# Kernel optimization log

Hardware: AMD Instinct MI355X
Metric: run time of the kernel (lower is better)

Reference implementation:

```python
import jax, jax.numpy as jnp
import numpy as np

L = 4096          # total packed tokens (B=1)
N_SEQ = 8         # number of packed sequences
SEQ = L // N_SEQ  # equal lengths of 512
H = 8
E = 64
NEG_BIAS = -10000.0  # matches torch.where(mask, 0, -10000.0)


def setup_inputs() -> dict:
    key = jax.random.key(0)
    kq, kk, kv = jax.random.split(key, 3)
    q = jax.random.normal(kq, (1, L, H, E), dtype=jnp.float32)
    k = jax.random.normal(kk, (1, L, H, E), dtype=jnp.float32)
    v = jax.random.normal(kv, (1, L, H, E), dtype=jnp.float32)
    # segment id per token; equivalent to lenghts=[512]*8 in the torch module
    seg_ids = (jnp.arange(L, dtype=jnp.int32) // SEQ).astype(jnp.int32)
    return {"q": q, "k": k, "v": v, "seg_ids": seg_ids}


def reference(q, k, v, seg_ids):
    # direct_attention: scores = (q @ k^T) * scale + block-diagonal bias; softmax; @ v
    scale = 1.0 / jnp.sqrt(jnp.asarray(E, dtype=q.dtype))
    # [B,H,L,L]
    scores = jnp.einsum('blhe,bmhe->bhlm', q, k) * scale
    # block-diagonal mask from segment ids (same as create_block_mask(lengths))
    same_block = seg_ids[:, None] == seg_ids[None, :]          # [L,L] bool
    bias = jnp.where(same_block, 0.0, NEG_BIAS).astype(q.dtype)  # additive bias, not -inf
    attn = jax.nn.softmax(scores + bias, axis=-1)
    out = jnp.einsum('bhlm,bmhe->blhe', attn, v)
    return out
```

## Files before the change

kernel.cpp:

```cpp
#include <hip/hip_runtime.h>
#include <cstdint>

#define NSEG 8
#define SEQ  512
#define NH   8
#define NE   64
#define KVB  64
#define QTILE 128
#define KVHALF 256
#define NCH 4
#define M2BIAS 24.0f
#define LOG2E  1.4426950408889634f
#define LDS_TOTAL 131072

typedef __attribute__((ext_vector_type(8)))  __bf16   bf16x8;
typedef __attribute__((ext_vector_type(16))) float    f32x16;
typedef __attribute__((ext_vector_type(4)))  uint32_t u32x4;

static __device__ __forceinline__ uint32_t cvtpk(float lo, float hi) {
    uint32_t r;
    asm("v_cvt_pk_bf16_f32 %0, %1, %2" : "=v"(r) : "v"(lo), "v"(hi));
    return r;
}
static __device__ __forceinline__ float exp2_fast(float x) {
    float r;
    asm("v_exp_f32 %0, %1" : "=v"(r) : "v"(x));
    return r;
}
static __device__ __forceinline__ f32x16 zero16() {
    f32x16 z;
#pragma unroll
    for (int i = 0; i < 16; ++i) z[i] = 0.0f;
    return z;
}

struct Pref {
    float4 k0, k1, k2, k3;
    float4 va0, va1, vb0, vb1;
};

static __device__ __forceinline__ void issue_loads(
    const float* __restrict__ kg, const float* __restrict__ vg,
    int kbase, int h, int tg, Pref& P)
{
    const int kr = tg >> 2, kc = (tg & 3) * 16;
    const float* ks = kg + (size_t)(kbase + kr) * (NH * NE) + h * NE + kc;
    P.k0 = *(const float4*)(ks);
    P.k1 = *(const float4*)(ks + 4);
    P.k2 = *(const float4*)(ks + 8);
    P.k3 = *(const float4*)(ks + 12);
    const int vr = (tg & 31) * 2, ve = (tg >> 5) * 8;
    const float* vs = vg + (size_t)(kbase + vr) * (NH * NE) + h * NE + ve;
    P.va0 = *(const float4*)(vs);
    P.va1 = *(const float4*)(vs + 4);
    P.vb0 = *(const float4*)(vs + NH * NE);
    P.vb1 = *(const float4*)(vs + NH * NE + 4);
}

static __device__ __forceinline__ void convert_store(
    char* ldsK, char* ldsV, int gc, int tg, const Pref& P)
{
    {
        const int kr = tg >> 2, kc2 = (tg & 3) * 32;
        const int swz = (kr & 7) << 4;
        char* dst = ldsK + gc * 8192 + kr * 128;
        u32x4 w0 = { cvtpk(P.k0.x, P.k0.y), cvtpk(P.k0.z, P.k0.w),
                     cvtpk(P.k1.x, P.k1.y), cvtpk(P.k1.z, P.k1.w) };
        u32x4 w1 = { cvtpk(P.k2.x, P.k2.y), cvtpk(P.k2.z, P.k2.w),
                     cvtpk(P.k3.x, P.k3.y), cvtpk(P.k3.z, P.k3.w) };
        *(u32x4*)(dst + ((kc2)      ^ swz)) = w0;
        *(u32x4*)(dst + ((kc2 + 16) ^ swz)) = w1;
    }
    {
        const int vr = (tg & 31) * 2, ve = (tg >> 5) * 8;
        float a[8] = { P.va0.x, P.va0.y, P.va0.z, P.va0.w,
                       P.va1.x, P.va1.y, P.va1.z, P.va1.w };
        float b[8] = { P.vb0.x, P.vb0.y, P.vb0.z, P.vb0.w,
                       P.vb1.x, P.vb1.y, P.vb1.z, P.vb1.w };
#pragma unroll
        for (int i = 0; i < 8; ++i) {
            const int e = ve + i;
            *(uint32_t*)(ldsV + e * 1024 + gc * 128 + ((vr * 2) ^ ((e & 7) << 4))) = cvtpk(a[i], b[i]);
        }
    }
}

__global__ __launch_bounds__(512, 2) void attn_fwd(
    const float* __restrict__ qg, const float* __restrict__ kg,
    const float* __restrict__ vg, float* __restrict__ outg)
{
    extern __shared__ __align__(16) char lds[];
    char* ldsK = lds;
    char* ldsV = lds + 65536;

    const int bid = blockIdx.x;
    const int seg = bid & 7;
    const int h   = (bid >> 3) & 7;
    const int qt  = bid >> 6;

    const int t    = threadIdx.x;
    const int lane = t & 63;
    const int wid  = t >> 6;
    const int wq   = wid & 3;
    const int kgp  = wid >> 2;
    const int tg   = t & 255;
    const int ql   = lane & 31;
    const int hi   = lane >> 5;

    const int qbase  = seg * SEQ + qt * QTILE + wq * 32;
    const int kvbase = seg * SEQ + kgp * KVHALF;
    const int gc0    = kgp * NCH;

    Pref Pa, Pb;
    issue_loads(kg, vg, kvbase,       h, tg, Pa);
    issue_loads(kg, vg, kvbase + KVB, h, tg, Pb);

    bf16x8 qf[4];
#pragma unroll
    for (int s = 0; s < 4; ++s) {
        const float* qp = qg + (size_t)(qbase + ql) * (NH * NE) + h * NE + s * 16 + hi * 8;
        float4 a = *(const float4*)qp;
        float4 b = *(const float4*)(qp + 4);
        u32x4 w = { cvtpk(a.x * 0.125f, a.y * 0.125f), cvtpk(a.z * 0.125f, a.w * 0.125f),
                    cvtpk(b.x * 0.125f, b.y * 0.125f), cvtpk(b.z * 0.125f, b.w * 0.125f) };
        qf[s] = __builtin_bit_cast(bf16x8, w);
    }

    convert_store(ldsK, ldsV, gc0 + 0, tg, Pa);
    issue_loads(kg, vg, kvbase + 2 * KVB, h, tg, Pa);
    convert_store(ldsK, ldsV, gc0 + 1, tg, Pb);
    issue_loads(kg, vg, kvbase + 3 * KVB, h, tg, Pb);
    convert_store(ldsK, ldsV, gc0 + 2, tg, Pa);
    convert_store(ldsK, ldsV, gc0 + 3, tg, Pb);
    __syncthreads();

    f32x16 o0 = zero16();
    f32x16 o1 = zero16();
    float lsum = 0.0f;

#pragma unroll 1
    for (int c = 0; c < NCH; ++c) {
        const int gc = gc0 + c;
        const char* bK = ldsK + gc * 8192;

        f32x16 sa = zero16();
        f32x16 sb = zero16();
#pragma unroll
        for (int s = 0; s < 4; ++s) {
            const int col = (s * 32 + hi * 16) ^ ((ql & 7) << 4);
            bf16x8 ka = *(const bf16x8*)(bK + ql * 128 + col);
            bf16x8 kb = *(const bf16x8*)(bK + (ql + 32) * 128 + col);
            sa = __builtin_amdgcn_mfma_f32_32x32x16_bf16(ka, qf[s], sa, 0, 0, 0);
            sb = __builtin_amdgcn_mfma_f32_32x32x16_bf16(kb, qf[s], sb, 0, 0, 0);
        }

#pragma unroll
        for (int r = 0; r < 16; ++r) {
            sa[r] = exp2_fast(fmaf(sa[r], LOG2E, -M2BIAS));
            sb[r] = exp2_fast(fmaf(sb[r], LOG2E, -M2BIAS));
        }
        float acc = 0.0f;
#pragma unroll
        for (int r = 0; r < 16; ++r) acc += sa[r] + sb[r];
        lsum += acc;

        uint32_t WA[2][4], WB[2][4];
#pragma unroll
        for (int r0 = 0; r0 < 4; ++r0) {
            WA[0][r0] = cvtpk(sa[4 * r0],     sa[4 * r0 + 1]);
            WB[0][r0] = cvtpk(sa[4 * r0 + 2], sa[4 * r0 + 3]);
            WA[1][r0] = cvtpk(sb[4 * r0],     sb[4 * r0 + 1]);
            WB[1][r0] = cvtpk(sb[4 * r0 + 2], sb[4 * r0 + 3]);
        }

#pragma unroll
        for (int ks = 0; ks < 4; ++ks) {
            const int kt = ks >> 1, g2 = (ks & 1) * 2;
            uint32_t Ua = hi ? WA[kt][g2 + 1] : WA[kt][g2];
            uint32_t Ub = hi ? WB[kt][g2 + 1] : WB[kt][g2];
            uint32_t Sa = hi ? WA[kt][g2]     : WA[kt][g2 + 1];
            uint32_t Sb = hi ? WB[kt][g2]     : WB[kt][g2 + 1];
            uint32_t Ra = __shfl_xor(Sa, 32);
            uint32_t Rb = __shfl_xor(Sb, 32);
            u32x4 pw = { hi ? Ra : Ua, hi ? Rb : Ub, hi ? Ua : Ra, hi ? Ub : Rb };
            bf16x8 pf = __builtin_bit_cast(bf16x8, pw);
            {
                const int e = ql;
                bf16x8 vb = *(const bf16x8*)(ldsV + e * 1024 + gc * 128 +
                                             ((ks * 32 + hi * 16) ^ ((e & 7) << 4)));
                o0 = __builtin_amdgcn_mfma_f32_32x32x16_bf16(pf, vb, o0, 0, 0, 0);
            }
            {
                const int e = 32 + ql;
                bf16x8 vb = *(const bf16x8*)(ldsV + e * 1024 + gc * 128 +
                                             ((ks * 32 + hi * 16) ^ ((e & 7) << 4)));
                o1 = __builtin_amdgcn_mfma_f32_32x32x16_bf16(pf, vb, o1, 0, 0, 0);
            }
        }
    }

    __syncthreads();
    float* ex = (float*)lds;
    if (kgp == 1) {
        float* p = ex + (size_t)(wq * 64 + lane) * 33;
#pragma unroll
        for (int r = 0; r < 16; ++r) { p[r] = o0[r]; p[16 + r] = o1[r]; }
        p[32] = lsum;
    }
    __syncthreads();
    if (kgp == 0) {
        const float* p = ex + (size_t)(wq * 64 + lane) * 33;
#pragma unroll
        for (int r = 0; r < 16; ++r) { o0[r] += p[r]; o1[r] += p[16 + r]; }
        lsum += p[32];

        const float ltot = lsum + __shfl_xor(lsum, 32);
        const float rinv = 1.0f / ltot;
#pragma unroll
        for (int r = 0; r < 16; ++r) {
            const int qlocal = (r & 3) + 8 * (r >> 2) + 4 * hi;
            const float scl = __shfl(rinv, qlocal);
            float* op = outg + (size_t)(qbase + qlocal) * (NH * NE) + h * NE + ql;
            op[0]  = o0[r] * scl;
            op[32] = o1[r] * scl;
        }
    }
}

extern "C" void kernel_launch(void* const* d_in, const int* in_sizes, int n_in,
                              void* d_out, int out_size, void* d_ws, size_t ws_size,
                              hipStream_t stream)
{
    (void)in_sizes; (void)n_in; (void)d_ws; (void)ws_size; (void)out_size;
    const float* q = (const float*)d_in[0];
    const float* k = (const float*)d_in[1];
    const float* v = (const float*)d_in[2];
    float* out = (float*)d_out;
    (void)hipFuncSetAttribute((const void*)attn_fwd,
                              hipFuncAttributeMaxDynamicSharedMemorySize, LDS_TOTAL);
    attn_fwd<<<dim3(NSEG * NH * (SEQ / QTILE)), dim3(512), LDS_TOTAL, stream>>>(q, k, v, out);
}
```

Before: 21.08 us.

## Split keys across four wave groups with 1024-thread blocks and single-shot loads

Doubles the block size to 1024 threads so four wave groups each handle a quarter of the 512 keys, halving the per-wave serial chunk loop. The staged, double-buffered K/V prefetch is replaced by one bulk load per thread into registers followed by a single LDS store. The final reduction now merges three partial outputs through LDS instead of one. This trades more register pressure and lower occupancy per CU for shorter per-wave critical paths, and the 12-group exchange region must still fit in LDS.

```diff
diff --git a/kernel.cpp b/kernel.cpp
--- a/kernel.cpp
+++ b/kernel.cpp
@@ -7,8 +7,9 @@
 #define NE   64
 #define KVB  64
 #define QTILE 128
-#define KVHALF 256
-#define NCH 4
+#define NKGP 4
+#define KEYS_PER_G (SEQ / NKGP)
+#define NCH (KEYS_PER_G / KVB)
 #define M2BIAS 24.0f
 #define LOG2E  1.4426950408889634f
 #define LDS_TOTAL 131072
@@ -34,58 +35,7 @@
     return z;
 }
 
-struct Pref {
-    float4 k0, k1, k2, k3;
-    float4 va0, va1, vb0, vb1;
-};
-
-static __device__ __forceinline__ void issue_loads(
-    const float* __restrict__ kg, const float* __restrict__ vg,
-    int kbase, int h, int tg, Pref& P)
-{
-    const int kr = tg >> 2, kc = (tg & 3) * 16;
-    const float* ks = kg + (size_t)(kbase + kr) * (NH * NE) + h * NE + kc;
-    P.k0 = *(const float4*)(ks);
-    P.k1 = *(const float4*)(ks + 4);
-    P.k2 = *(const float4*)(ks + 8);
-    P.k3 = *(const float4*)(ks + 12);
-    const int vr = (tg & 31) * 2, ve = (tg >> 5) * 8;
-    const float* vs = vg + (size_t)(kbase + vr) * (NH * NE) + h * NE + ve;
-    P.va0 = *(const float4*)(vs);
-    P.va1 = *(const float4*)(vs + 4);
-    P.vb0 = *(const float4*)(vs + NH * NE);
-    P.vb1 = *(const float4*)(vs + NH * NE + 4);
-}
-
-static __device__ __forceinline__ void convert_store(
-    char* ldsK, char* ldsV, int gc, int tg, const Pref& P)
-{
-    {
-        const int kr = tg >> 2, kc2 = (tg & 3) * 32;
-        const int swz = (kr & 7) << 4;
-        char* dst = ldsK + gc * 8192 + kr * 128;
-        u32x4 w0 = { cvtpk(P.k0.x, P.k0.y), cvtpk(P.k0.z, P.k0.w),
-                     cvtpk(P.k1.x, P.k1.y), cvtpk(P.k1.z, P.k1.w) };
-        u32x4 w1 = { cvtpk(P.k2.x, P.k2.y), cvtpk(P.k2.z, P.k2.w),
-                     cvtpk(P.k3.x, P.k3.y), cvtpk(P.k3.z, P.k3.w) };
-        *(u32x4*)(dst + ((kc2)      ^ swz)) = w0;
-        *(u32x4*)(dst + ((kc2 + 16) ^ swz)) = w1;
-    }
-    {
-        const int vr = (tg & 31) * 2, ve = (tg >> 5) * 8;
-        float a[8] = { P.va0.x, P.va0.y, P.va0.z, P.va0.w,
-                       P.va1.x, P.va1.y, P.va1.z, P.va1.w };
-        float b[8] = { P.vb0.x, P.vb0.y, P.vb0.z, P.vb0.w,
-                       P.vb1.x, P.vb1.y, P.vb1.z, P.vb1.w };
-#pragma unroll
-        for (int i = 0; i < 8; ++i) {
-            const int e = ve + i;
-            *(uint32_t*)(ldsV + e * 1024 + gc * 128 + ((vr * 2) ^ ((e & 7) << 4))) = cvtpk(a[i], b[i]);
-        }
-    }
-}
-
-__global__ __launch_bounds__(512, 2) void attn_fwd(
+__global__ __launch_bounds__(1024) void attn_fwd(
     const float* __restrict__ qg, const float* __restrict__ kg,
     const float* __restrict__ vg, float* __restrict__ outg)
 {
@@ -103,17 +53,26 @@
     const int wid  = t >> 6;
     const int wq   = wid & 3;
     const int kgp  = wid >> 2;
-    const int tg   = t & 255;
     const int ql   = lane & 31;
     const int hi   = lane >> 5;
 
-    const int qbase  = seg * SEQ + qt * QTILE + wq * 32;
-    const int kvbase = seg * SEQ + kgp * KVHALF;
-    const int gc0    = kgp * NCH;
-
-    Pref Pa, Pb;
-    issue_loads(kg, vg, kvbase,       h, tg, Pa);
-    issue_loads(kg, vg, kvbase + KVB, h, tg, Pb);
+    const int qbase = seg * SEQ + qt * QTILE + wq * 32;
+    const int kvseg = seg * SEQ;
+
+    const int kr = t >> 1, kc = (t & 1) * 32;
+    const float* ksrc = kg + (size_t)(kvseg + kr) * (NH * NE) + h * NE + kc;
+    float4 KL[8];
+#pragma unroll
+    for (int j = 0; j < 8; ++j) KL[j] = *(const float4*)(ksrc + j * 4);
+
+    const int kp = t >> 2, ve = (t & 3) * 16;
+    const float* vsrc = vg + (size_t)(kvseg + kp * 2) * (NH * NE) + h * NE + ve;
+    float4 VA[4], VB[4];
+#pragma unroll
+    for (int j = 0; j < 4; ++j) {
+        VA[j] = *(const float4*)(vsrc + j * 4);
+        VB[j] = *(const float4*)(vsrc + NH * NE + j * 4);
+    }
 
     bf16x8 qf[4];
 #pragma unroll
@@ -126,12 +85,30 @@
         qf[s] = __builtin_bit_cast(bf16x8, w);
     }
 
-    convert_store(ldsK, ldsV, gc0 + 0, tg, Pa);
-    issue_loads(kg, vg, kvbase + 2 * KVB, h, tg, Pa);
-    convert_store(ldsK, ldsV, gc0 + 1, tg, Pb);
-    issue_loads(kg, vg, kvbase + 3 * KVB, h, tg, Pb);
-    convert_store(ldsK, ldsV, gc0 + 2, tg, Pa);
-    convert_store(ldsK, ldsV, gc0 + 3, tg, Pb);
+    {
+        const int kc2 = (t & 1) * 64;
+        const int swz = (kr & 7) << 4;
+        char* dst = ldsK + kr * 128;
+#pragma unroll
+        for (int j = 0; j < 4; ++j) {
+            u32x4 w = { cvtpk(KL[2 * j].x,     KL[2 * j].y),
+                        cvtpk(KL[2 * j].z,     KL[2 * j].w),
+                        cvtpk(KL[2 * j + 1].x, KL[2 * j + 1].y),
+                        cvtpk(KL[2 * j + 1].z, KL[2 * j + 1].w) };
+            *(u32x4*)(dst + ((kc2 + j * 16) ^ swz)) = w;
+        }
+    }
+    {
+        float a[16] = { VA[0].x, VA[0].y, VA[0].z, VA[0].w, VA[1].x, VA[1].y, VA[1].z, VA[1].w,
+                        VA[2].x, VA[2].y, VA[2].z, VA[2].w, VA[3].x, VA[3].y, VA[3].z, VA[3].w };
+        float b[16] = { VB[0].x, VB[0].y, VB[0].z, VB[0].w, VB[1].x, VB[1].y, VB[1].z, VB[1].w,
+                        VB[2].x, VB[2].y, VB[2].z, VB[2].w, VB[3].x, VB[3].y, VB[3].z, VB[3].w };
+#pragma unroll
+        for (int i = 0; i < 16; ++i) {
+            const int e = ve + i;
+            *(uint32_t*)(ldsV + e * 1024 + ((kp * 4) ^ ((e & 7) << 4))) = cvtpk(a[i], b[i]);
+        }
+    }
     __syncthreads();
 
     f32x16 o0 = zero16();
@@ -140,7 +117,7 @@
 
 #pragma unroll 1
     for (int c = 0; c < NCH; ++c) {
-        const int gc = gc0 + c;
+        const int gc = kgp * NCH + c;
         const char* bK = ldsK + gc * 8192;
 
         f32x16 sa = zero16();
@@ -201,18 +178,21 @@
 
     __syncthreads();
     float* ex = (float*)lds;
-    if (kgp == 1) {
-        float* p = ex + (size_t)(wq * 64 + lane) * 33;
+    if (kgp != 0) {
+        float* p = ex + (size_t)(((kgp - 1) * 4 + wq) * 64 + lane) * 33;
 #pragma unroll
         for (int r = 0; r < 16; ++r) { p[r] = o0[r]; p[16 + r] = o1[r]; }
         p[32] = lsum;
     }
     __syncthreads();
     if (kgp == 0) {
-        const float* p = ex + (size_t)(wq * 64 + lane) * 33;
-#pragma unroll
-        for (int r = 0; r < 16; ++r) { o0[r] += p[r]; o1[r] += p[16 + r]; }
-        lsum += p[32];
+#pragma unroll
+        for (int g = 0; g < 3; ++g) {
+            const float* p = ex + (size_t)((g * 4 + wq) * 64 + lane) * 33;
+#pragma unroll
+            for (int r = 0; r < 16; ++r) { o0[r] += p[r]; o1[r] += p[16 + r]; }
+            lsum += p[32];
+        }
 
         const float ltot = lsum + __shfl_xor(lsum, 32);
         const float rinv = 1.0f / ltot;
@@ -238,5 +218,5 @@
     float* out = (float*)d_out;
     (void)hipFuncSetAttribute((const void*)attn_fwd,
                               hipFuncAttributeMaxDynamicSharedMemorySize, LDS_TOTAL);
-    attn_fwd<<<dim3(NSEG * NH * (SEQ / QTILE)), dim3(512), LDS_TOTAL, stream>>>(q, k, v, out);
-}
+    attn_fwd<<<dim3(NSEG * NH * (SEQ / QTILE)), dim3(1024), LDS_TOTAL, stream>>>(q, k, v, out);
+}
```

Result: slower. 23.35 us (+10.8%).
